# Kernel optimization log

Measured on AMD Instinct MI355X. Metric: run time of the kernel, lower is better.

The kernel has to match this reference:

```python
import jax, jax.numpy as jnp
import numpy as np
from jax import lax

B, S, H, E, TOP_K = 4, 2048, 8192, 256, 8

def setup_inputs() -> dict:
    key = jax.random.key(0)
    kx, kw = jax.random.split(key)
    x = jax.random.normal(kx, (B, S, H), dtype=jnp.float32)
    # Dense kernel init scale ~ 1/sqrt(H)
    W_router = jax.random.normal(kw, (H, E), dtype=jnp.float32) * (1.0 / np.sqrt(H))
    return {"x": x, "W_router": W_router}

def reference(x, W_router):
    # router_logits: [B, S, E]
    router_logits = jnp.einsum('bsh,he->bse', x, W_router)
    top_logits, top_indices = lax.top_k(router_logits, k=TOP_K)  # [B,S,K]
    routing_weights = jax.nn.softmax(top_logits, axis=-1)        # [B,S,K]
    return routing_weights, top_indices, router_logits
```

## Files before the change

### kernel.cpp

```cpp
#include <hip/hip_runtime.h>
#include <math.h>
#include <float.h>

typedef _Float16 half8 __attribute__((ext_vector_type(8)));
typedef float f32x4 __attribute__((ext_vector_type(4)));

namespace {
constexpr int kH = 8192, kE = 256, kTopK = 8, kTok = 8192;
constexpr int kIdxOff = kTok * kTopK;
constexpr int kLogitsOff = 2 * kTok * kTopK;
constexpr int kBM = 128, kBN = 128, kBK = 32;
constexpr int kPadH = 40;
constexpr int kCand = 16;
constexpr float kEps = 5e-5f;
constexpr float kInvScale = 1.0f / 262144.0f;
constexpr size_t kWtF   = (size_t)kE * kH;
constexpr size_t kWtlF  = kWtF + (size_t)kE * kH / 2;
constexpr size_t kPartF = kWtF + (size_t)kE * kH;
constexpr size_t kPartStride = (size_t)kTok * kE;
}

__device__ __forceinline__ void gld16(const _Float16* g, _Float16* l) {
    __builtin_amdgcn_global_load_lds(
        (const __attribute__((address_space(1))) void*)g,
        (__attribute__((address_space(3))) void*)l, 16, 0, 0);
}

__global__ __launch_bounds__(1024)
void prep_w(const float* __restrict__ W, float* __restrict__ Wt,
            _Float16* __restrict__ Wth, _Float16* __restrict__ Wtl) {
    __shared__ float tile[32][33];
    const int k0 = blockIdx.x * 32, e0 = blockIdx.y * 32;
    const int tx = threadIdx.x, ty = threadIdx.y;
    tile[ty][tx] = W[(size_t)(k0 + ty) * kE + (e0 + tx)];
    __syncthreads();
    const float v = tile[tx][ty];
    const size_t o = (size_t)(e0 + ty) * kH + (k0 + tx);
    Wt[o] = v;
    const float vs = v * 256.0f;
    const _Float16 h = (_Float16)vs;
    Wth[o] = h;
    Wtl[o] = (_Float16)(vs - (float)h);
}

__global__ __launch_bounds__(256, 2)
void router_gemm_mfma(const float* __restrict__ x,
                      const _Float16* __restrict__ Wth,
                      const _Float16* __restrict__ Wtl,
                      float* __restrict__ p0, float* __restrict__ pws,
                      int kchunk)
{
    __shared__ __align__(16) _Float16 sxh[2][kBM * kPadH];
    __shared__ __align__(16) _Float16 sxl[2][kBM * kPadH];
    __shared__ __align__(16) _Float16 swh[2][kBN * kBK];
    __shared__ __align__(16) _Float16 swl[2][kBN * kBK];

    const int tid  = threadIdx.x;
    const int lane = tid & 63;
    const int w    = tid >> 6;
    const int wm   = w >> 1, wn = w & 1;
    const int t0   = blockIdx.x * kBM;
    const int e0   = blockIdx.y * kBN;
    const int kbase = blockIdx.z * kchunk;
    const int nsteps = kchunk / kBK;

    f32x4 acc[4][4];
    #pragma unroll
    for (int m = 0; m < 4; ++m)
        #pragma unroll
        for (int n = 0; n < 4; ++n) {
            acc[m][n][0] = 0.f; acc[m][n][1] = 0.f;
            acc[m][n][2] = 0.f; acc[m][n][3] = 0.f;
        }

    const size_t wro0 = (size_t)(e0 + (w << 4) + (lane >> 2)) * kH
                        + kbase + ((lane & 3) << 3);
    const size_t wro1 = wro0 + (size_t)64 * kH;
    const int wl0 = (w << 9);
    const int wl1 = (w << 9) + 2048;

    const int srow = tid >> 1;
    const int scg  = (tid & 1) << 4;
    const float* xp = x + (size_t)(t0 + srow) * kH + kbase + scg;

    float4 xr0, xr1, xr2, xr3;

#define CVT_STORE(B)                                                           \
    {                                                                          \
        float xf[16];                                                          \
        xf[0]=xr0.x; xf[1]=xr0.y; xf[2]=xr0.z; xf[3]=xr0.w;                    \
        xf[4]=xr1.x; xf[5]=xr1.y; xf[6]=xr1.z; xf[7]=xr1.w;                    \
        xf[8]=xr2.x; xf[9]=xr2.y; xf[10]=xr2.z; xf[11]=xr2.w;                  \
        xf[12]=xr3.x; xf[13]=xr3.y; xf[14]=xr3.z; xf[15]=xr3.w;                \
        half8 h0, h1, l0, l1;                                                  \
        _Pragma("unroll")                                                      \
        for (int i = 0; i < 8; ++i) {                                          \
            const float sA = xf[i] * 1024.0f;                                  \
            const _Float16 hA = (_Float16)sA;                                  \
            h0[i] = hA; l0[i] = (_Float16)(sA - (float)hA);                    \
            const float sB = xf[i + 8] * 1024.0f;                              \
            const _Float16 hB = (_Float16)sB;                                  \
            h1[i] = hB; l1[i] = (_Float16)(sB - (float)hB);                    \
        }                                                                      \
        *reinterpret_cast<half8*>(&sxh[B][srow * kPadH + scg])     = h0;       \
        *reinterpret_cast<half8*>(&sxh[B][srow * kPadH + scg + 8]) = h1;       \
        *reinterpret_cast<half8*>(&sxl[B][srow * kPadH + scg])     = l0;       \
        *reinterpret_cast<half8*>(&sxl[B][srow * kPadH + scg + 8]) = l1;       \
    }

    gld16(Wth + wro0, &swh[0][wl0]);
    gld16(Wth + wro1, &swh[0][wl1]);
    gld16(Wtl + wro0, &swl[0][wl0]);
    gld16(Wtl + wro1, &swl[0][wl1]);
    xr0 = *reinterpret_cast<const float4*>(xp);
    xr1 = *reinterpret_cast<const float4*>(xp + 4);
    xr2 = *reinterpret_cast<const float4*>(xp + 8);
    xr3 = *reinterpret_cast<const float4*>(xp + 12);
    CVT_STORE(0)
    if (nsteps > 1) {
        xr0 = *reinterpret_cast<const float4*>(xp + 32);
        xr1 = *reinterpret_cast<const float4*>(xp + 36);
        xr2 = *reinterpret_cast<const float4*>(xp + 40);
        xr3 = *reinterpret_cast<const float4*>(xp + 44);
    }
    __syncthreads();

    const int fr = lane & 15;
    const int fk = (lane >> 4) << 3;

    for (int t = 0; t < nsteps; ++t) {
        const int cur = t & 1, nxt = cur ^ 1;

        if (t + 1 < nsteps) {
            const size_t ko = (size_t)(t + 1) << 5;
            gld16(Wth + wro0 + ko, &swh[nxt][wl0]);
            gld16(Wth + wro1 + ko, &swh[nxt][wl1]);
            gld16(Wtl + wro0 + ko, &swl[nxt][wl0]);
            gld16(Wtl + wro1 + ko, &swl[nxt][wl1]);
            CVT_STORE(nxt)
            if (t + 2 < nsteps) {
                const float* nx = xp + ((size_t)(t + 2) << 5);
                xr0 = *reinterpret_cast<const float4*>(nx);
                xr1 = *reinterpret_cast<const float4*>(nx + 4);
                xr2 = *reinterpret_cast<const float4*>(nx + 8);
                xr3 = *reinterpret_cast<const float4*>(nx + 12);
            }
        }

        half8 ah[4], al[4];
        #pragma unroll
        for (int m = 0; m < 4; ++m) {
            const int arow = (wm << 6) + (m << 4) + fr;
            ah[m] = *reinterpret_cast<const half8*>(&sxh[cur][arow * kPadH + fk]);
            al[m] = *reinterpret_cast<const half8*>(&sxl[cur][arow * kPadH + fk]);
        }
        #pragma unroll
        for (int n = 0; n < 4; ++n) {
            const int brow = (wn << 6) + (n << 4) + fr;
            const half8 bh = *reinterpret_cast<const half8*>(&swh[cur][brow * kBK + fk]);
            const half8 bl = *reinterpret_cast<const half8*>(&swl[cur][brow * kBK + fk]);
            #pragma unroll
            for (int m = 0; m < 4; ++m) {
                acc[m][n] = __builtin_amdgcn_mfma_f32_16x16x32_f16(ah[m], bh, acc[m][n], 0, 0, 0);
                acc[m][n] = __builtin_amdgcn_mfma_f32_16x16x32_f16(ah[m], bl, acc[m][n], 0, 0, 0);
                acc[m][n] = __builtin_amdgcn_mfma_f32_16x16x32_f16(al[m], bh, acc[m][n], 0, 0, 0);
            }
        }

        __syncthreads();
    }
#undef CVT_STORE

    float* dst = (blockIdx.z == 0) ? p0 : (pws + (size_t)(blockIdx.z - 1) * kPartStride);
    const int r0 = (lane >> 4) << 2;
    const int c0 = lane & 15;
    #pragma unroll
    for (int m = 0; m < 4; ++m)
        #pragma unroll
        for (int n = 0; n < 4; ++n) {
            const int col = e0 + (wn << 6) + (n << 4) + c0;
            #pragma unroll
            for (int r = 0; r < 4; ++r) {
                const int row = t0 + (wm << 6) + (m << 4) + r0 + r;
                dst[(size_t)row * kE + col] = acc[m][n][r] * kInvScale;
            }
        }
}

#define ARGMAX_ROUND(r)                                                        \
    {                                                                          \
        float bv = v0; int bi = (lane << 2);                                   \
        if (v1 > bv) { bv = v1; bi = (lane << 2) + 1; }                        \
        if (v2 > bv) { bv = v2; bi = (lane << 2) + 2; }                        \
        if (v3 > bv) { bv = v3; bi = (lane << 2) + 3; }                        \
        _Pragma("unroll")                                                      \
        for (int off = 32; off > 0; off >>= 1) {                               \
            const float ov = __shfl_xor(bv, off, 64);                          \
            const int   oi = __shfl_xor(bi, off, 64);                          \
            if (ov > bv || (ov == bv && oi < bi)) { bv = ov; bi = oi; }        \
        }                                                                      \
        if (lane == (r)) { myv = bv; myi = bi; }                               \
        if ((bi >> 2) == lane) {                                               \
            const int m = bi & 3;                                              \
            if      (m == 0) v0 = -FLT_MAX;                                    \
            else if (m == 1) v1 = -FLT_MAX;                                    \
            else if (m == 2) v2 = -FLT_MAX;                                    \
            else             v3 = -FLT_MAX;                                    \
        }                                                                      \
    }

__global__ __launch_bounds__(256)
void combine_select(const float* __restrict__ x, const float* __restrict__ Wt,
                    const float* __restrict__ pws, float* __restrict__ out,
                    int npart)
{
    const int lane = threadIdx.x & 63;
    const int w    = threadIdx.x >> 6;
    const int row  = blockIdx.x * 4 + w;
    float* logits = out + kLogitsOff;
    const size_t rb = (size_t)row * kE + (lane << 2);

    float4 s = *reinterpret_cast<const float4*>(logits + rb);
    for (int p = 0; p < npart; ++p) {
        const float4 q = *reinterpret_cast<const float4*>(pws + (size_t)p * kPartStride + rb);
        s.x += q.x; s.y += q.y; s.z += q.z; s.w += q.w;
    }
    *reinterpret_cast<float4*>(logits + rb) = s;

    float v0 = s.x, v1 = s.y, v2 = s.z, v3 = s.w;
    float myv = -FLT_MAX; int myi = -1;

    #pragma unroll
    for (int r = 0; r < 9; ++r) ARGMAX_ROUND(r)

    const float nv = __shfl_down(myv, 1, 64);
    const unsigned long long amb = __ballot(lane < 8 && (myv - nv) < kEps);

    if (amb == 0ull) {
        const float m = __shfl(myv, 0, 64);
        const float e = (lane < kTopK) ? expf(myv - m) : 0.f;
        float t = e;
        #pragma unroll
        for (int off = 1; off < 8; off <<= 1) t += __shfl_xor(t, off, 64);
        if (lane < kTopK) {
            out[(size_t)row * kTopK + lane]           = e / t;
            out[kIdxOff + (size_t)row * kTopK + lane] = (float)myi;
        }
    } else {
        #pragma unroll
        for (int r = 9; r < kCand; ++r) ARGMAX_ROUND(r)

        const float* xr = x + (size_t)row * kH;
        double dv = -1.0e300;
        #pragma unroll 1
        for (int cg = 0; cg < kCand; cg += 4) {
            const int i0 = __shfl(myi, cg + 0, 64);
            const int i1 = __shfl(myi, cg + 1, 64);
            const int i2 = __shfl(myi, cg + 2, 64);
            const int i3 = __shfl(myi, cg + 3, 64);
            const float* w0 = Wt + (size_t)i0 * kH;
            const float* w1 = Wt + (size_t)i1 * kH;
            const float* w2 = Wt + (size_t)i2 * kH;
            const float* w3 = Wt + (size_t)i3 * kH;
            double a0 = 0.0, a1 = 0.0, a2 = 0.0, a3 = 0.0;
            for (int k = (lane << 2); k < kH; k += 256) {
                const float4 xv = *reinterpret_cast<const float4*>(xr + k);
                const float4 q0 = *reinterpret_cast<const float4*>(w0 + k);
                const float4 q1 = *reinterpret_cast<const float4*>(w1 + k);
                const float4 q2 = *reinterpret_cast<const float4*>(w2 + k);
                const float4 q3 = *reinterpret_cast<const float4*>(w3 + k);
                a0 = fma((double)xv.x, (double)q0.x, a0);
                a1 = fma((double)xv.x, (double)q1.x, a1);
                a2 = fma((double)xv.x, (double)q2.x, a2);
                a3 = fma((double)xv.x, (double)q3.x, a3);
                a0 = fma((double)xv.y, (double)q0.y, a0);
                a1 = fma((double)xv.y, (double)q1.y, a1);
                a2 = fma((double)xv.y, (double)q2.y, a2);
                a3 = fma((double)xv.y, (double)q3.y, a3);
                a0 = fma((double)xv.z, (double)q0.z, a0);
                a1 = fma((double)xv.z, (double)q1.z, a1);
                a2 = fma((double)xv.z, (double)q2.z, a2);
                a3 = fma((double)xv.z, (double)q3.z, a3);
                a0 = fma((double)xv.w, (double)q0.w, a0);
                a1 = fma((double)xv.w, (double)q1.w, a1);
                a2 = fma((double)xv.w, (double)q2.w, a2);
                a3 = fma((double)xv.w, (double)q3.w, a3);
            }
            #pragma unroll
            for (int off = 32; off > 0; off >>= 1) {
                a0 += __shfl_xor(a0, off, 64);
                a1 += __shfl_xor(a1, off, 64);
                a2 += __shfl_xor(a2, off, 64);
                a3 += __shfl_xor(a3, off, 64);
            }
            if (lane == cg + 0) dv = a0;
            if (lane == cg + 1) dv = a1;
            if (lane == cg + 2) dv = a2;
            if (lane == cg + 3) dv = a3;
        }

        double cv = dv; int ci = myi;
        double mx = 0.0, ssum = 0.0, keepv = 0.0; int keepi = 0;
        #pragma unroll 1
        for (int r = 0; r < kTopK; ++r) {
            double bv = cv; int bi = ci;
            #pragma unroll
            for (int off = 32; off > 0; off >>= 1) {
                const double ov = __shfl_xor(bv, off, 64);
                const int    oi = __shfl_xor(bi, off, 64);
                if (ov > bv || (ov == bv && oi < bi)) { bv = ov; bi = oi; }
            }
            if (r == 0) mx = bv;
            ssum += exp(bv - mx);
            if (lane == r) { keepv = bv; keepi = bi; }
            if (ci == bi) cv = -1.0e300;
        }
        if (lane < kTopK) {
            out[(size_t)row * kTopK + lane]           = (float)(exp(keepv - mx) / ssum);
            out[kIdxOff + (size_t)row * kTopK + lane] = (float)keepi;
        }
    }
}

extern "C" void kernel_launch(void* const* d_in, const int* in_sizes, int n_in,
                              void* d_out, int out_size, void* d_ws, size_t ws_size,
                              hipStream_t stream) {
    const float* x  = (const float*)d_in[0];
    const float* Wr = (const float*)d_in[1];
    float* out = (float*)d_out;
    float* Wt  = (float*)d_ws;
    _Float16* Wth = (_Float16*)((float*)d_ws + kWtF);
    _Float16* Wtl = (_Float16*)((float*)d_ws + kWtlF);
    float* pws = (float*)d_ws + kPartF;
    (void)in_sizes; (void)n_in; (void)out_size;

    const size_t need4 = (kPartF + 3 * kPartStride) * sizeof(float);
    const int nkc = (ws_size >= need4) ? 4 : 2;
    const int kchunk = kH / nkc;

    hipLaunchKernelGGL(prep_w, dim3(kH / 32, kE / 32), dim3(32, 32), 0, stream,
                       Wr, Wt, Wth, Wtl);
    hipLaunchKernelGGL(router_gemm_mfma, dim3(kTok / kBM, kE / kBN, nkc), dim3(256),
                       0, stream, x, Wth, Wtl, out + kLogitsOff, pws, kchunk);
    hipLaunchKernelGGL(combine_select, dim3(kTok / 4), dim3(256), 0, stream,
                       x, Wt, pws, out, nkc - 1);
}
```

Before: 230.3 us.

## Load W fragments directly into registers and single-buffer the X tile in LDS

The weight hi/lo tiles are no longer staged in LDS through global_load_lds. Each wave now loads its MFMA B fragments straight from global memory into registers, double-buffered in registers across two unrolled steps. The X tile drops to a single LDS buffer, with two barriers per k-step around the convert/store and compute phases. This saves LDS and avoids LDS reads for B. In exchange, W global loads become redundant across the wm waves, register pressure rises, and the extra barriers per step add synchronisation cost.

```diff
diff --git a/kernel.cpp b/kernel.cpp
--- a/kernel.cpp
+++ b/kernel.cpp
@@ -18,12 +18,6 @@
 constexpr size_t kWtlF  = kWtF + (size_t)kE * kH / 2;
 constexpr size_t kPartF = kWtF + (size_t)kE * kH;
 constexpr size_t kPartStride = (size_t)kTok * kE;
-}
-
-__device__ __forceinline__ void gld16(const _Float16* g, _Float16* l) {
-    __builtin_amdgcn_global_load_lds(
-        (const __attribute__((address_space(1))) void*)g,
-        (__attribute__((address_space(3))) void*)l, 16, 0, 0);
 }
 
 __global__ __launch_bounds__(1024)
@@ -50,10 +44,8 @@
                       float* __restrict__ p0, float* __restrict__ pws,
                       int kchunk)
 {
-    __shared__ __align__(16) _Float16 sxh[2][kBM * kPadH];
-    __shared__ __align__(16) _Float16 sxl[2][kBM * kPadH];
-    __shared__ __align__(16) _Float16 swh[2][kBN * kBK];
-    __shared__ __align__(16) _Float16 swl[2][kBN * kBK];
+    __shared__ __align__(16) _Float16 sxh[kBM * kPadH];
+    __shared__ __align__(16) _Float16 sxl[kBM * kPadH];
 
     const int tid  = threadIdx.x;
     const int lane = tid & 63;
@@ -64,6 +56,9 @@
     const int kbase = blockIdx.z * kchunk;
     const int nsteps = kchunk / kBK;
 
+    const int fr = lane & 15;
+    const int fk = (lane >> 4) << 3;
+
     f32x4 acc[4][4];
     #pragma unroll
     for (int m = 0; m < 4; ++m)
@@ -73,103 +68,105 @@
             acc[m][n][2] = 0.f; acc[m][n][3] = 0.f;
         }
 
-    const size_t wro0 = (size_t)(e0 + (w << 4) + (lane >> 2)) * kH
-                        + kbase + ((lane & 3) << 3);
-    const size_t wro1 = wro0 + (size_t)64 * kH;
-    const int wl0 = (w << 9);
-    const int wl1 = (w << 9) + 2048;
-
     const int srow = tid >> 1;
     const int scg  = (tid & 1) << 4;
     const float* xp = x + (size_t)(t0 + srow) * kH + kbase + scg;
 
-    float4 xr0, xr1, xr2, xr3;
-
-#define CVT_STORE(B)                                                           \
+    const size_t wro = (size_t)(e0 + (wn << 6) + fr) * kH + kbase + fk;
+    const _Float16* whb = Wth + wro;
+    const _Float16* wlb = Wtl + wro;
+
+#define LOAD_X(D0, D1, D2, D3, T)                                              \
+    {                                                                          \
+        const float* p_ = xp + ((size_t)(T) << 5);                             \
+        D0 = *reinterpret_cast<const float4*>(p_);                             \
+        D1 = *reinterpret_cast<const float4*>(p_ + 4);                         \
+        D2 = *reinterpret_cast<const float4*>(p_ + 8);                         \
+        D3 = *reinterpret_cast<const float4*>(p_ + 12);                        \
+    }
+
+#define LOAD_W(WH, WL, T)                                                      \
+    {                                                                          \
+        _Pragma("unroll")                                                      \
+        for (int n_ = 0; n_ < 4; ++n_) {                                       \
+            const size_t o_ = (size_t)n_ * ((size_t)16 * kH)                   \
+                              + ((size_t)(T) << 5);                            \
+            WH[n_] = *reinterpret_cast<const half8*>(whb + o_);                \
+            WL[n_] = *reinterpret_cast<const half8*>(wlb + o_);                \
+        }                                                                      \
+    }
+
+#define CVT_STORE(X0, X1, X2, X3)                                              \
     {                                                                          \
         float xf[16];                                                          \
-        xf[0]=xr0.x; xf[1]=xr0.y; xf[2]=xr0.z; xf[3]=xr0.w;                    \
-        xf[4]=xr1.x; xf[5]=xr1.y; xf[6]=xr1.z; xf[7]=xr1.w;                    \
-        xf[8]=xr2.x; xf[9]=xr2.y; xf[10]=xr2.z; xf[11]=xr2.w;                  \
-        xf[12]=xr3.x; xf[13]=xr3.y; xf[14]=xr3.z; xf[15]=xr3.w;                \
+        xf[0]=X0.x; xf[1]=X0.y; xf[2]=X0.z; xf[3]=X0.w;                        \
+        xf[4]=X1.x; xf[5]=X1.y; xf[6]=X1.z; xf[7]=X1.w;                        \
+        xf[8]=X2.x; xf[9]=X2.y; xf[10]=X2.z; xf[11]=X2.w;                      \
+        xf[12]=X3.x; xf[13]=X3.y; xf[14]=X3.z; xf[15]=X3.w;                    \
         half8 h0, h1, l0, l1;                                                  \
         _Pragma("unroll")                                                      \
-        for (int i = 0; i < 8; ++i) {                                          \
-            const float sA = xf[i] * 1024.0f;                                  \
+        for (int i_ = 0; i_ < 8; ++i_) {                                       \
+            const float sA = xf[i_] * 1024.0f;                                 \
             const _Float16 hA = (_Float16)sA;                                  \
-            h0[i] = hA; l0[i] = (_Float16)(sA - (float)hA);                    \
-            const float sB = xf[i + 8] * 1024.0f;                              \
+            h0[i_] = hA; l0[i_] = (_Float16)(sA - (float)hA);                  \
+            const float sB = xf[i_ + 8] * 1024.0f;                             \
             const _Float16 hB = (_Float16)sB;                                  \
-            h1[i] = hB; l1[i] = (_Float16)(sB - (float)hB);                    \
-        }                                                                      \
-        *reinterpret_cast<half8*>(&sxh[B][srow * kPadH + scg])     = h0;       \
-        *reinterpret_cast<half8*>(&sxh[B][srow * kPadH + scg + 8]) = h1;       \
-        *reinterpret_cast<half8*>(&sxl[B][srow * kPadH + scg])     = l0;       \
-        *reinterpret_cast<half8*>(&sxl[B][srow * kPadH + scg + 8]) = l1;       \
-    }
-
-    gld16(Wth + wro0, &swh[0][wl0]);
-    gld16(Wth + wro1, &swh[0][wl1]);
-    gld16(Wtl + wro0, &swl[0][wl0]);
-    gld16(Wtl + wro1, &swl[0][wl1]);
-    xr0 = *reinterpret_cast<const float4*>(xp);
-    xr1 = *reinterpret_cast<const float4*>(xp + 4);
-    xr2 = *reinterpret_cast<const float4*>(xp + 8);
-    xr3 = *reinterpret_cast<const float4*>(xp + 12);
-    CVT_STORE(0)
-    if (nsteps > 1) {
-        xr0 = *reinterpret_cast<const float4*>(xp + 32);
-        xr1 = *reinterpret_cast<const float4*>(xp + 36);
-        xr2 = *reinterpret_cast<const float4*>(xp + 40);
-        xr3 = *reinterpret_cast<const float4*>(xp + 44);
-    }
-    __syncthreads();
-
-    const int fr = lane & 15;
-    const int fk = (lane >> 4) << 3;
-
-    for (int t = 0; t < nsteps; ++t) {
-        const int cur = t & 1, nxt = cur ^ 1;
-
-        if (t + 1 < nsteps) {
-            const size_t ko = (size_t)(t + 1) << 5;
-            gld16(Wth + wro0 + ko, &swh[nxt][wl0]);
-            gld16(Wth + wro1 + ko, &swh[nxt][wl1]);
-            gld16(Wtl + wro0 + ko, &swl[nxt][wl0]);
-            gld16(Wtl + wro1 + ko, &swl[nxt][wl1]);
-            CVT_STORE(nxt)
-            if (t + 2 < nsteps) {
-                const float* nx = xp + ((size_t)(t + 2) << 5);
-                xr0 = *reinterpret_cast<const float4*>(nx);
-                xr1 = *reinterpret_cast<const float4*>(nx + 4);
-                xr2 = *reinterpret_cast<const float4*>(nx + 8);
-                xr3 = *reinterpret_cast<const float4*>(nx + 12);
-            }
-        }
-
-        half8 ah[4], al[4];
-        #pragma unroll
-        for (int m = 0; m < 4; ++m) {
-            const int arow = (wm << 6) + (m << 4) + fr;
-            ah[m] = *reinterpret_cast<const half8*>(&sxh[cur][arow * kPadH + fk]);
-            al[m] = *reinterpret_cast<const half8*>(&sxl[cur][arow * kPadH + fk]);
-        }
-        #pragma unroll
-        for (int n = 0; n < 4; ++n) {
-            const int brow = (wn << 6) + (n << 4) + fr;
-            const half8 bh = *reinterpret_cast<const half8*>(&swh[cur][brow * kBK + fk]);
-            const half8 bl = *reinterpret_cast<const half8*>(&swl[cur][brow * kBK + fk]);
-            #pragma unroll
-            for (int m = 0; m < 4; ++m) {
-                acc[m][n] = __builtin_amdgcn_mfma_f32_16x16x32_f16(ah[m], bh, acc[m][n], 0, 0, 0);
-                acc[m][n] = __builtin_amdgcn_mfma_f32_16x16x32_f16(ah[m], bl, acc[m][n], 0, 0, 0);
-                acc[m][n] = __builtin_amdgcn_mfma_f32_16x16x32_f16(al[m], bh, acc[m][n], 0, 0, 0);
-            }
-        }
-
+            h1[i_] = hB; l1[i_] = (_Float16)(sB - (float)hB);                  \
+        }                                                                      \
+        *reinterpret_cast<half8*>(&sxh[srow * kPadH + scg])     = h0;          \
+        *reinterpret_cast<half8*>(&sxh[srow * kPadH + scg + 8]) = h1;          \
+        *reinterpret_cast<half8*>(&sxl[srow * kPadH + scg])     = l0;          \
+        *reinterpret_cast<half8*>(&sxl[srow * kPadH + scg + 8]) = l1;          \
+    }
+
+#define COMPUTE(WH, WL)                                                        \
+    {                                                                          \
+        half8 ah[4], al[4];                                                    \
+        _Pragma("unroll")                                                      \
+        for (int m_ = 0; m_ < 4; ++m_) {                                       \
+            const int arow = (wm << 6) + (m_ << 4) + fr;                       \
+            ah[m_] = *reinterpret_cast<const half8*>(&sxh[arow * kPadH + fk]); \
+            al[m_] = *reinterpret_cast<const half8*>(&sxl[arow * kPadH + fk]); \
+        }                                                                      \
+        _Pragma("unroll")                                                      \
+        for (int n_ = 0; n_ < 4; ++n_)                                         \
+            _Pragma("unroll")                                                  \
+            for (int m_ = 0; m_ < 4; ++m_) {                                   \
+                acc[m_][n_] = __builtin_amdgcn_mfma_f32_16x16x32_f16(          \
+                    ah[m_], WH[n_], acc[m_][n_], 0, 0, 0);                     \
+                acc[m_][n_] = __builtin_amdgcn_mfma_f32_16x16x32_f16(          \
+                    ah[m_], WL[n_], acc[m_][n_], 0, 0, 0);                     \
+                acc[m_][n_] = __builtin_amdgcn_mfma_f32_16x16x32_f16(          \
+                    al[m_], WH[n_], acc[m_][n_], 0, 0, 0);                     \
+            }                                                                  \
+    }
+
+    float4 xA0, xA1, xA2, xA3, xB0, xB1, xB2, xB3;
+    half8 whA[4], wlA[4], whB[4], wlB[4];
+
+    LOAD_X(xA0, xA1, xA2, xA3, 0)
+    LOAD_W(whA, wlA, 0)
+    LOAD_X(xB0, xB1, xB2, xB3, 1)
+
+    for (int t = 0; t < nsteps; t += 2) {
+        LOAD_W(whB, wlB, t + 1)
+        CVT_STORE(xA0, xA1, xA2, xA3)
         __syncthreads();
-    }
+        if (t + 2 < nsteps) LOAD_X(xA0, xA1, xA2, xA3, t + 2)
+        COMPUTE(whA, wlA)
+        __syncthreads();
+
+        if (t + 2 < nsteps) LOAD_W(whA, wlA, t + 2)
+        CVT_STORE(xB0, xB1, xB2, xB3)
+        __syncthreads();
+        if (t + 3 < nsteps) LOAD_X(xB0, xB1, xB2, xB3, t + 3)
+        COMPUTE(whB, wlB)
+        __syncthreads();
+    }
+#undef LOAD_X
+#undef LOAD_W
 #undef CVT_STORE
+#undef COMPUTE
 
     float* dst = (blockIdx.z == 0) ? p0 : (pws + (size_t)(blockIdx.z - 1) * kPartStride);
     const int r0 = (lane >> 4) << 2;
```

After: 254.8 us. 1.11x slower.
